# Optimization experiments

Measured on AMD Instinct MI355X. Metric: run time of the kernel, lower is better.

The kernel has to match this reference:

```python
import jax, jax.numpy as jnp
import numpy as np
from jax.scipy.special import logsumexp

S, L = 32768, 512  # seq_len, label_num


def setup_inputs() -> dict:
    key = jax.random.key(0)
    k1, k2, k3 = jax.random.split(key, 3)
    logit = jax.random.normal(k1, (S, L), dtype=jnp.float32)   # emissions [S, L]
    labels = jax.random.randint(k2, (S,), 0, L)                # gold path [S]
    T = jax.random.normal(k3, (L, L), dtype=jnp.float32)       # T[next, prev]
    return {"logit": logit, "labels": labels, "T": T}


def _crf_loss(logit, T, labels):
    # Forward algorithm: alpha_t[j] = logsumexp_i(alpha_{t-1}[i] + T[j, i]) + feat_t[j]
    alpha0 = logit[0]

    def step(alpha, feat):
        new_alpha = logsumexp(alpha[None, :] + T, axis=1) + feat  # [L]
        return new_alpha, None

    alpha_final, _ = jax.lax.scan(step, alpha0, logit[1:])
    log_Z = logsumexp(alpha_final)

    # Gold path score: feat_0[y0] + sum_{t>0} (feat_t[y_t] + T[y_t, y_{t-1}])
    emit = logit[0, labels[0]] + jnp.sum(logit[jnp.arange(1, logit.shape[0]), labels[1:]])
    trans = jnp.sum(T[labels[1:], labels[:-1]])
    gold = emit + trans
    return log_Z - gold


def reference(logit, labels, T):
    return _crf_loss(logit, T, labels)
```

## Files before the change

kernel.cpp:

```cpp
#include <hip/hip_runtime.h>
#include <stdint.h>


#define S_LEN 32768
#define L 512
#define CH 16
#define NCF 2048
#define WGF 128
#define WGB 128
#define LN448 6.104793232f
#define LN2   0.6931471806f

#define OFF_EAF  0
#define OFF_EAB  (256*1024)
#define OFF_G    (512*1024)
#define OFF_H    (OFF_G + 2048*512*2)
#define OFF_LSE  (OFF_H + 2048*512*2)
#define OFF_GOLD (OFF_LSE + 4104*4)

typedef float v4f __attribute__((ext_vector_type(4)));

__device__ __forceinline__ float b2f(unsigned short u){
  return __uint_as_float(((unsigned)u) << 16);
}
__device__ __forceinline__ unsigned short f2b(float x){
  unsigned u = __float_as_uint(x);
  return (unsigned short)((u + 0x7fffu + ((u >> 16) & 1u)) >> 16);
}
__device__ __forceinline__ unsigned char to_fp8(float v){
  int u = __builtin_amdgcn_cvt_pk_fp8_f32(v, v, 0, false);
  return (unsigned char)(u & 0xff);
}

extern "C" __global__ void crf_prep(const float* __restrict__ T,
                                    unsigned char* __restrict__ EAf,
                                    unsigned char* __restrict__ EAb){
  int tid = blockIdx.x*512 + threadIdx.x;
  int r    = tid & 7;
  int lane = (tid >> 3) & 63;
  int kt   = (tid >> 9) & 15;
  int mtw  = tid >> 13;
  int j = (mtw >> 2)*64 + (mtw & 3)*16 + (lane & 15);
  int i = kt*32 + ((lane >> 4) << 3) + r;
  EAf[tid] = to_fp8(2.0f * __expf(T[j*L + i]));
  EAb[tid] = to_fp8(2.0f * __expf(T[i*L + j]));
}

extern "C" __global__ __launch_bounds__(512, 2)
void crf_chunks(const float* __restrict__ logit,
                const unsigned char* __restrict__ EAf,
                const unsigned char* __restrict__ EAb,
                unsigned short* __restrict__ G, unsigned short* __restrict__ H){
  __shared__ __align__(16) unsigned char Pl[2][8192];
  __shared__ float sPart[16][8];

  const int tid  = threadIdx.x;
  const int w    = tid >> 6;
  const int lane = tid & 63;
  const int quad = lane >> 4;
  const int cl   = lane & 15;
  const bool fwd = (blockIdx.x < WGF);
  const int  b   = fwd ? blockIdx.x : (blockIdx.x - WGF);
  const int  cg  = fwd ? (b*16 + cl) : (1 + b*16 + cl);
  const int  cgc = min(cg, NCF-1);
  const bool isc0 = fwd && (cg == 0);
  const int  jrow0 = w*64 + quad*4;

  const long* EA = (const long*)(fwd ? EAf : EAb);
  long eA[4][16];
  #pragma unroll
  for (int mt = 0; mt < 4; ++mt)
    #pragma unroll
    for (int kt = 0; kt < 16; ++kt)
      eA[mt][kt] = EA[(((w<<2)+mt)<<4 | kt)*64 + lane];

  float vr[4][4];
  if (fwd) {
    #pragma unroll
    for (int mt = 0; mt < 4; ++mt)
      #pragma unroll
      for (int r = 0; r < 4; ++r) vr[mt][r] = 1.0f;
  } else {
    const int t0 = cgc*CH + CH - 1;
    const float* lp = logit + (size_t)t0*L + jrow0;
    #pragma unroll
    for (int mt = 0; mt < 4; ++mt) {
      float4 x = *(const float4*)(lp + mt*16);
      vr[mt][0] = __expf(x.x); vr[mt][1] = __expf(x.y);
      vr[mt][2] = __expf(x.z); vr[mt][3] = __expf(x.w);
    }
  }
  float m = 0.0f;
  int par = 0;

  auto renorm_store = [&](int dst){
    float mx = vr[0][0];
    #pragma unroll
    for (int mt = 0; mt < 4; ++mt)
      #pragma unroll
      for (int r = 0; r < 4; ++r) mx = fmaxf(mx, vr[mt][r]);
    mx = fmaxf(mx, __shfl_xor(mx, 16));
    mx = fmaxf(mx, __shfl_xor(mx, 32));
    if (quad == 0) sPart[cl][w] = mx;
    __syncthreads();
    float4 pa = *(const float4*)&sPart[cl][0];
    float4 pb = *(const float4*)&sPart[cl][4];
    float M = fmaxf(fmaxf(fmaxf(pa.x,pa.y),fmaxf(pa.z,pa.w)),
                    fmaxf(fmaxf(pb.x,pb.y),fmaxf(pb.z,pb.w)));
    float sc = 448.0f / M;
    #pragma unroll
    for (int mt = 0; mt < 4; ++mt) {
      int u = __builtin_amdgcn_cvt_pk_fp8_f32(vr[mt][0]*sc, vr[mt][1]*sc, 0, false);
      u     = __builtin_amdgcn_cvt_pk_fp8_f32(vr[mt][2]*sc, vr[mt][3]*sc, u, true);
      int r0 = jrow0 + mt*16;
      *(int*)&Pl[dst][(r0 >> 5)*512 + ((((r0 >> 3) & 3)*16 + cl) << 3) + (r0 & 7)] = u;
    }
    m += __logf(M) - LN448;
    __syncthreads();
  };

  renorm_store(0);

  for (int k = 0; k < CH; ++k) {
    const bool last = (k == CH-1);
    const bool useF = fwd || !last;

    v4f acc[4];
    #pragma unroll
    for (int mt = 0; mt < 4; ++mt) acc[mt] = (v4f){0.f,0.f,0.f,0.f};
    #pragma unroll
    for (int kt = 0; kt < 16; ++kt) {
      long bb = *(const long*)&Pl[par][kt*512 + lane*8];
      #pragma unroll
      for (int mt = 0; mt < 4; ++mt)
        acc[mt] = __builtin_amdgcn_mfma_f32_16x16x32_fp8_fp8(eA[mt][kt], bb, acc[mt], 0, 0, 0);
    }
    m -= LN2;

    if (useF) {
      const int t = fwd ? (cgc*CH + k) : (cgc*CH + CH - 2 - k);
      const float* lp = logit + (size_t)t*L + jrow0;
      #pragma unroll
      for (int mt = 0; mt < 4; ++mt) {
        float4 x = *(const float4*)(lp + mt*16);
        float f0 = __expf(x.x), f1 = __expf(x.y), f2 = __expf(x.z), f3 = __expf(x.w);
        vr[mt][0] = acc[mt][0]*f0; vr[mt][1] = acc[mt][1]*f1;
        vr[mt][2] = acc[mt][2]*f2; vr[mt][3] = acc[mt][3]*f3;
        if (k == 0 && isc0) {
          vr[mt][0] = f0; vr[mt][1] = f1; vr[mt][2] = f2; vr[mt][3] = f3;
        }
      }
      if (k == 0 && isc0) m = 0.0f;
    } else {
      #pragma unroll
      for (int mt = 0; mt < 4; ++mt)
        #pragma unroll
        for (int r = 0; r < 4; ++r) vr[mt][r] = acc[mt][r];
    }

    if (last) {
      if (cg <= NCF-1) {
        unsigned short* dst = (fwd ? G : H) + (size_t)cg*L + jrow0;
        #pragma unroll
        for (int mt = 0; mt < 4; ++mt) {
          ushort4 o;
          o.x = f2b(__logf(vr[mt][0]) + m); o.y = f2b(__logf(vr[mt][1]) + m);
          o.z = f2b(__logf(vr[mt][2]) + m); o.w = f2b(__logf(vr[mt][3]) + m);
          *(ushort4*)(dst + mt*16) = o;
        }
      }
    } else {
      renorm_store(par ^ 1);
      par ^= 1;
    }
  }
}

__device__ __forceinline__ float blockMax(float v, float* sred){
  #pragma unroll
  for (int off = 32; off >= 1; off >>= 1) v = fmaxf(v, __shfl_xor(v, off));
  int wid = threadIdx.x >> 6, lane = threadIdx.x & 63;
  if (lane == 0) sred[wid] = v;
  __syncthreads();
  if (threadIdx.x < 8) {
    float t = sred[threadIdx.x];
    t = fmaxf(t, __shfl_xor(t, 4));
    t = fmaxf(t, __shfl_xor(t, 2));
    t = fmaxf(t, __shfl_xor(t, 1));
    if (threadIdx.x == 0) sred[15] = t;
  }
  __syncthreads();
  float r = sred[15];
  __syncthreads();
  return r;
}
__device__ __forceinline__ float blockSum(float v, float* sred){
  #pragma unroll
  for (int off = 32; off >= 1; off >>= 1) v += __shfl_xor(v, off);
  int wid = threadIdx.x >> 6, lane = threadIdx.x & 63;
  if (lane == 0) sred[wid] = v;
  __syncthreads();
  if (threadIdx.x < 8) {
    float t = sred[threadIdx.x];
    t += __shfl_xor(t, 4); t += __shfl_xor(t, 2); t += __shfl_xor(t, 1);
    if (threadIdx.x == 0) sred[15] = t;
  }
  __syncthreads();
  float r = sred[15];
  __syncthreads();
  return r;
}

extern "C" __global__ __launch_bounds__(512)
void crf_lse(const unsigned short* __restrict__ G,
             const unsigned short* __restrict__ H,
             float* __restrict__ lsebuf){
  __shared__ float sred[16];
  int j = threadIdx.x, b = blockIdx.x;
  if (b == 0) {
    float v = b2f(G[(size_t)(NCF-1)*L + j]);
    float M = blockMax(v, sred);
    float ss = blockSum(__expf(v - M), sred);
    if (j == 0) lsebuf[2*NCF] = M + __logf(ss);
  } else {
    int c = b;
    float h = b2f(H[(size_t)c*L + j]);
    float g = b2f(G[(size_t)(c-1)*L + j]);
    float v1 = h + g;
    float M1 = blockMax(v1, sred);
    float s1 = blockSum(__expf(v1 - M1), sred);
    float M2 = blockMax(h, sred);
    float s2 = blockSum(__expf(h - M2), sred);
    if (j == 0) { lsebuf[c] = M1 + __logf(s1); lsebuf[NCF + c] = M2 + __logf(s2); }
  }
}

extern "C" __global__ void crf_gold(const float* __restrict__ logit,
                                    const int* __restrict__ labels,
                                    const float* __restrict__ T,
                                    float* __restrict__ part){
  __shared__ float sred[8];
  int tid = threadIdx.x;
  float acc = 0.f;
  for (int t = blockIdx.x*256 + tid; t < S_LEN; t += gridDim.x*256) {
    int yt = labels[t];
    float v = logit[(size_t)t*L + yt];
    if (t > 0) v += T[yt*L + labels[t-1]];
    acc += v;
  }
  #pragma unroll
  for (int off = 32; off >= 1; off >>= 1) acc += __shfl_xor(acc, off);
  int wid = tid >> 6, lane = tid & 63;
  if (lane == 0) sred[wid] = acc;
  __syncthreads();
  if (tid == 0) part[blockIdx.x] = sred[0] + sred[1] + sred[2] + sred[3];
}

extern "C" __global__ __launch_bounds__(512)
void crf_final(const float* __restrict__ lsebuf,
               const float* __restrict__ part,
               float* __restrict__ out){
  __shared__ float sred[16];
  int j = threadIdx.x;
  float acc = 0.f;
  #pragma unroll
  for (int c = j; c < NCF; c += 512)
    if (c >= 1) acc += lsebuf[c] - lsebuf[NCF + c];
  if (j < 64) acc -= part[j];
  float s = blockSum(acc, sred);
  if (j == 0) out[0] = lsebuf[2*NCF] + s;
}

extern "C" void kernel_launch(void* const* d_in, const int* in_sizes, int n_in,
                              void* d_out, int out_size, void* d_ws, size_t ws_size,
                              hipStream_t stream){
  const float* logit = (const float*)d_in[0];
  const int* labels  = (const int*)d_in[1];
  const float* T     = (const float*)d_in[2];
  float* out = (float*)d_out;
  char* ws = (char*)d_ws;
  unsigned char* EAf = (unsigned char*)(ws + OFF_EAF);
  unsigned char* EAb = (unsigned char*)(ws + OFF_EAB);
  unsigned short* G  = (unsigned short*)(ws + OFF_G);
  unsigned short* H  = (unsigned short*)(ws + OFF_H);
  float* lsebuf = (float*)(ws + OFF_LSE);
  float* part   = (float*)(ws + OFF_GOLD);

  crf_prep  <<<512, 512, 0, stream>>>(T, EAf, EAb);
  crf_chunks<<<WGF + WGB, 512, 0, stream>>>(logit, EAf, EAb, G, H);
  crf_lse   <<<NCF, 512, 0, stream>>>(G, H, lsebuf);
  crf_gold  <<<64, 256, 0, stream>>>(logit, labels, T, part);
  crf_final <<<1, 512, 0, stream>>>(lsebuf, part, out);
}
```

Before: 148.8 us.

## Fuse CRF pipeline into one persistent kernel with grid barriers

```diff
diff --git a/kernel.cpp b/kernel.cpp
--- a/kernel.cpp
+++ b/kernel.cpp
@@ -6,8 +6,7 @@
 #define L 512
 #define CH 16
 #define NCF 2048
-#define WGF 128
-#define WGB 128
+#define NB  256
 #define LN448 6.104793232f
 #define LN2   0.6931471806f
 
@@ -17,6 +16,7 @@
 #define OFF_H    (OFF_G + 2048*512*2)
 #define OFF_LSE  (OFF_H + 2048*512*2)
 #define OFF_GOLD (OFF_LSE + 4104*4)
+#define OFF_BAR  (OFF_GOLD + 1024)
 
 typedef float v4f __attribute__((ext_vector_type(4)));
 
@@ -32,168 +32,17 @@
   return (unsigned char)(u & 0xff);
 }
 
-extern "C" __global__ void crf_prep(const float* __restrict__ T,
-                                    unsigned char* __restrict__ EAf,
-                                    unsigned char* __restrict__ EAb){
-  int tid = blockIdx.x*512 + threadIdx.x;
-  int r    = tid & 7;
-  int lane = (tid >> 3) & 63;
-  int kt   = (tid >> 9) & 15;
-  int mtw  = tid >> 13;
-  int j = (mtw >> 2)*64 + (mtw & 3)*16 + (lane & 15);
-  int i = kt*32 + ((lane >> 4) << 3) + r;
-  EAf[tid] = to_fp8(2.0f * __expf(T[j*L + i]));
-  EAb[tid] = to_fp8(2.0f * __expf(T[i*L + j]));
-}
-
-extern "C" __global__ __launch_bounds__(512, 2)
-void crf_chunks(const float* __restrict__ logit,
-                const unsigned char* __restrict__ EAf,
-                const unsigned char* __restrict__ EAb,
-                unsigned short* __restrict__ G, unsigned short* __restrict__ H){
-  __shared__ __align__(16) unsigned char Pl[2][8192];
-  __shared__ float sPart[16][8];
-
-  const int tid  = threadIdx.x;
-  const int w    = tid >> 6;
-  const int lane = tid & 63;
-  const int quad = lane >> 4;
-  const int cl   = lane & 15;
-  const bool fwd = (blockIdx.x < WGF);
-  const int  b   = fwd ? blockIdx.x : (blockIdx.x - WGF);
-  const int  cg  = fwd ? (b*16 + cl) : (1 + b*16 + cl);
-  const int  cgc = min(cg, NCF-1);
-  const bool isc0 = fwd && (cg == 0);
-  const int  jrow0 = w*64 + quad*4;
-
-  const long* EA = (const long*)(fwd ? EAf : EAb);
-  long eA[4][16];
-  #pragma unroll
-  for (int mt = 0; mt < 4; ++mt)
-    #pragma unroll
-    for (int kt = 0; kt < 16; ++kt)
-      eA[mt][kt] = EA[(((w<<2)+mt)<<4 | kt)*64 + lane];
-
-  float vr[4][4];
-  if (fwd) {
-    #pragma unroll
-    for (int mt = 0; mt < 4; ++mt)
-      #pragma unroll
-      for (int r = 0; r < 4; ++r) vr[mt][r] = 1.0f;
-  } else {
-    const int t0 = cgc*CH + CH - 1;
-    const float* lp = logit + (size_t)t0*L + jrow0;
-    #pragma unroll
-    for (int mt = 0; mt < 4; ++mt) {
-      float4 x = *(const float4*)(lp + mt*16);
-      vr[mt][0] = __expf(x.x); vr[mt][1] = __expf(x.y);
-      vr[mt][2] = __expf(x.z); vr[mt][3] = __expf(x.w);
-    }
-  }
-  float m = 0.0f;
-  int par = 0;
-
-  auto renorm_store = [&](int dst){
-    float mx = vr[0][0];
-    #pragma unroll
-    for (int mt = 0; mt < 4; ++mt)
-      #pragma unroll
-      for (int r = 0; r < 4; ++r) mx = fmaxf(mx, vr[mt][r]);
-    mx = fmaxf(mx, __shfl_xor(mx, 16));
-    mx = fmaxf(mx, __shfl_xor(mx, 32));
-    if (quad == 0) sPart[cl][w] = mx;
-    __syncthreads();
-    float4 pa = *(const float4*)&sPart[cl][0];
-    float4 pb = *(const float4*)&sPart[cl][4];
-    float M = fmaxf(fmaxf(fmaxf(pa.x,pa.y),fmaxf(pa.z,pa.w)),
-                    fmaxf(fmaxf(pb.x,pb.y),fmaxf(pb.z,pb.w)));
-    float sc = 448.0f / M;
-    #pragma unroll
-    for (int mt = 0; mt < 4; ++mt) {
-      int u = __builtin_amdgcn_cvt_pk_fp8_f32(vr[mt][0]*sc, vr[mt][1]*sc, 0, false);
-      u     = __builtin_amdgcn_cvt_pk_fp8_f32(vr[mt][2]*sc, vr[mt][3]*sc, u, true);
-      int r0 = jrow0 + mt*16;
-      *(int*)&Pl[dst][(r0 >> 5)*512 + ((((r0 >> 3) & 3)*16 + cl) << 3) + (r0 & 7)] = u;
-    }
-    m += __logf(M) - LN448;
-    __syncthreads();
-  };
-
-  renorm_store(0);
-
-  for (int k = 0; k < CH; ++k) {
-    const bool last = (k == CH-1);
-    const bool useF = fwd || !last;
-
-    v4f acc[4];
-    #pragma unroll
-    for (int mt = 0; mt < 4; ++mt) acc[mt] = (v4f){0.f,0.f,0.f,0.f};
-    #pragma unroll
-    for (int kt = 0; kt < 16; ++kt) {
-      long bb = *(const long*)&Pl[par][kt*512 + lane*8];
-      #pragma unroll
-      for (int mt = 0; mt < 4; ++mt)
-        acc[mt] = __builtin_amdgcn_mfma_f32_16x16x32_fp8_fp8(eA[mt][kt], bb, acc[mt], 0, 0, 0);
-    }
-    m -= LN2;
-
-    if (useF) {
-      const int t = fwd ? (cgc*CH + k) : (cgc*CH + CH - 2 - k);
-      const float* lp = logit + (size_t)t*L + jrow0;
-      #pragma unroll
-      for (int mt = 0; mt < 4; ++mt) {
-        float4 x = *(const float4*)(lp + mt*16);
-        float f0 = __expf(x.x), f1 = __expf(x.y), f2 = __expf(x.z), f3 = __expf(x.w);
-        vr[mt][0] = acc[mt][0]*f0; vr[mt][1] = acc[mt][1]*f1;
-        vr[mt][2] = acc[mt][2]*f2; vr[mt][3] = acc[mt][3]*f3;
-        if (k == 0 && isc0) {
-          vr[mt][0] = f0; vr[mt][1] = f1; vr[mt][2] = f2; vr[mt][3] = f3;
-        }
-      }
-      if (k == 0 && isc0) m = 0.0f;
-    } else {
-      #pragma unroll
-      for (int mt = 0; mt < 4; ++mt)
-        #pragma unroll
-        for (int r = 0; r < 4; ++r) vr[mt][r] = acc[mt][r];
-    }
-
-    if (last) {
-      if (cg <= NCF-1) {
-        unsigned short* dst = (fwd ? G : H) + (size_t)cg*L + jrow0;
-        #pragma unroll
-        for (int mt = 0; mt < 4; ++mt) {
-          ushort4 o;
-          o.x = f2b(__logf(vr[mt][0]) + m); o.y = f2b(__logf(vr[mt][1]) + m);
-          o.z = f2b(__logf(vr[mt][2]) + m); o.w = f2b(__logf(vr[mt][3]) + m);
-          *(ushort4*)(dst + mt*16) = o;
-        }
-      }
-    } else {
-      renorm_store(par ^ 1);
-      par ^= 1;
-    }
-  }
-}
-
-__device__ __forceinline__ float blockMax(float v, float* sred){
-  #pragma unroll
-  for (int off = 32; off >= 1; off >>= 1) v = fmaxf(v, __shfl_xor(v, off));
-  int wid = threadIdx.x >> 6, lane = threadIdx.x & 63;
-  if (lane == 0) sred[wid] = v;
-  __syncthreads();
-  if (threadIdx.x < 8) {
-    float t = sred[threadIdx.x];
-    t = fmaxf(t, __shfl_xor(t, 4));
-    t = fmaxf(t, __shfl_xor(t, 2));
-    t = fmaxf(t, __shfl_xor(t, 1));
-    if (threadIdx.x == 0) sred[15] = t;
-  }
-  __syncthreads();
-  float r = sred[15];
-  __syncthreads();
-  return r;
-}
+__device__ __forceinline__ void grid_bar(unsigned* bar, unsigned target){
+  __syncthreads();
+  if (threadIdx.x == 0) {
+    __threadfence();
+    __hip_atomic_fetch_add(bar, 1u, __ATOMIC_RELEASE, __HIP_MEMORY_SCOPE_AGENT);
+    while (__hip_atomic_load(bar, __ATOMIC_ACQUIRE, __HIP_MEMORY_SCOPE_AGENT) < target)
+      __builtin_amdgcn_s_sleep(2);
+  }
+  __syncthreads();
+}
+
 __device__ __forceinline__ float blockSum(float v, float* sred){
   #pragma unroll
   for (int off = 32; off >= 1; off >>= 1) v += __shfl_xor(v, off);
@@ -211,64 +60,246 @@
   return r;
 }
 
-extern "C" __global__ __launch_bounds__(512)
-void crf_lse(const unsigned short* __restrict__ G,
-             const unsigned short* __restrict__ H,
-             float* __restrict__ lsebuf){
-  __shared__ float sred[16];
-  int j = threadIdx.x, b = blockIdx.x;
-  if (b == 0) {
-    float v = b2f(G[(size_t)(NCF-1)*L + j]);
-    float M = blockMax(v, sred);
-    float ss = blockSum(__expf(v - M), sred);
-    if (j == 0) lsebuf[2*NCF] = M + __logf(ss);
-  } else {
-    int c = b;
-    float h = b2f(H[(size_t)c*L + j]);
-    float g = b2f(G[(size_t)(c-1)*L + j]);
-    float v1 = h + g;
-    float M1 = blockMax(v1, sred);
-    float s1 = blockSum(__expf(v1 - M1), sred);
-    float M2 = blockMax(h, sred);
-    float s2 = blockSum(__expf(h - M2), sred);
-    if (j == 0) { lsebuf[c] = M1 + __logf(s1); lsebuf[NCF + c] = M2 + __logf(s2); }
-  }
-}
-
-extern "C" __global__ void crf_gold(const float* __restrict__ logit,
-                                    const int* __restrict__ labels,
-                                    const float* __restrict__ T,
-                                    float* __restrict__ part){
-  __shared__ float sred[8];
-  int tid = threadIdx.x;
-  float acc = 0.f;
-  for (int t = blockIdx.x*256 + tid; t < S_LEN; t += gridDim.x*256) {
-    int yt = labels[t];
-    float v = logit[(size_t)t*L + yt];
-    if (t > 0) v += T[yt*L + labels[t-1]];
-    acc += v;
-  }
+__device__ __forceinline__ float waveMax(float v){
   #pragma unroll
-  for (int off = 32; off >= 1; off >>= 1) acc += __shfl_xor(acc, off);
-  int wid = tid >> 6, lane = tid & 63;
-  if (lane == 0) sred[wid] = acc;
-  __syncthreads();
-  if (tid == 0) part[blockIdx.x] = sred[0] + sred[1] + sred[2] + sred[3];
-}
-
-extern "C" __global__ __launch_bounds__(512)
-void crf_final(const float* __restrict__ lsebuf,
-               const float* __restrict__ part,
-               float* __restrict__ out){
-  __shared__ float sred[16];
-  int j = threadIdx.x;
-  float acc = 0.f;
+  for (int off = 32; off >= 1; off >>= 1) v = fmaxf(v, __shfl_xor(v, off));
+  return v;
+}
+__device__ __forceinline__ float waveSum(float v){
   #pragma unroll
-  for (int c = j; c < NCF; c += 512)
-    if (c >= 1) acc += lsebuf[c] - lsebuf[NCF + c];
-  if (j < 64) acc -= part[j];
-  float s = blockSum(acc, sred);
-  if (j == 0) out[0] = lsebuf[2*NCF] + s;
+  for (int off = 32; off >= 1; off >>= 1) v += __shfl_xor(v, off);
+  return v;
+}
+
+extern "C" __global__ __launch_bounds__(512, 2)
+void crf_fused(const float* __restrict__ logit,
+               const int* __restrict__ labels,
+               const float* __restrict__ T,
+               float* __restrict__ out,
+               unsigned char* __restrict__ EAf,
+               unsigned char* __restrict__ EAb,
+               unsigned short* __restrict__ G,
+               unsigned short* __restrict__ H,
+               float* __restrict__ lsebuf,
+               float* __restrict__ part,
+               unsigned* __restrict__ bar){
+  __shared__ __align__(16) unsigned char Pl[2][8192];
+  __shared__ float sPart[16][8];
+  __shared__ float sredG[16];
+
+  const int tidx = threadIdx.x;
+
+  for (int tid = blockIdx.x*512 + tidx; tid < 262144; tid += NB*512) {
+    int r    = tid & 7;
+    int lane = (tid >> 3) & 63;
+    int kt   = (tid >> 9) & 15;
+    int mtw  = tid >> 13;
+    int j = (mtw >> 2)*64 + (mtw & 3)*16 + (lane & 15);
+    int i = kt*32 + ((lane >> 4) << 3) + r;
+    EAf[tid] = to_fp8(2.0f * __expf(T[j*L + i]));
+    EAb[tid] = to_fp8(2.0f * __expf(T[i*L + j]));
+  }
+  {
+    float acc = 0.f;
+    if (tidx < 128) {
+      int t = blockIdx.x*128 + tidx;
+      int yt = labels[t];
+      float v = logit[(size_t)t*L + yt];
+      if (t > 0) v += T[yt*L + labels[t-1]];
+      acc = v;
+    }
+    float s = blockSum(acc, sredG);
+    if (tidx == 0) part[blockIdx.x] = s;
+  }
+  grid_bar(bar, NB);
+
+  {
+    const int w    = tidx >> 6;
+    const int lane = tidx & 63;
+    const int quad = lane >> 4;
+    const int cl   = lane & 15;
+    const bool fwd = (blockIdx.x < NB/2);
+    const int  b   = fwd ? blockIdx.x : (blockIdx.x - NB/2);
+    const int  cg  = fwd ? (b*16 + cl) : (1 + b*16 + cl);
+    const int  cgc = min(cg, NCF-1);
+    const bool isc0 = fwd && (cg == 0);
+    const int  jrow0 = w*64 + quad*4;
+
+    const long* EA = (const long*)(fwd ? EAf : EAb);
+    long eA[4][16];
+    #pragma unroll
+    for (int mt = 0; mt < 4; ++mt)
+      #pragma unroll
+      for (int kt = 0; kt < 16; ++kt)
+        eA[mt][kt] = EA[(((w<<2)+mt)<<4 | kt)*64 + lane];
+
+    float vr[4][4];
+    if (fwd) {
+      #pragma unroll
+      for (int mt = 0; mt < 4; ++mt)
+        #pragma unroll
+        for (int r = 0; r < 4; ++r) vr[mt][r] = 1.0f;
+    } else {
+      const int t0 = cgc*CH + CH - 1;
+      const float* lp = logit + (size_t)t0*L + jrow0;
+      #pragma unroll
+      for (int mt = 0; mt < 4; ++mt) {
+        float4 x = *(const float4*)(lp + mt*16);
+        vr[mt][0] = __expf(x.x); vr[mt][1] = __expf(x.y);
+        vr[mt][2] = __expf(x.z); vr[mt][3] = __expf(x.w);
+      }
+    }
+    float m = 0.0f;
+    int par = 0;
+
+    auto renorm_store = [&](int dst){
+      float mx = vr[0][0];
+      #pragma unroll
+      for (int mt = 0; mt < 4; ++mt)
+        #pragma unroll
+        for (int r = 0; r < 4; ++r) mx = fmaxf(mx, vr[mt][r]);
+      mx = fmaxf(mx, __shfl_xor(mx, 16));
+      mx = fmaxf(mx, __shfl_xor(mx, 32));
+      if (quad == 0) sPart[cl][w] = mx;
+      __syncthreads();
+      float4 pa = *(const float4*)&sPart[cl][0];
+      float4 pb = *(const float4*)&sPart[cl][4];
+      float M = fmaxf(fmaxf(fmaxf(pa.x,pa.y),fmaxf(pa.z,pa.w)),
+                      fmaxf(fmaxf(pb.x,pb.y),fmaxf(pb.z,pb.w)));
+      float sc = 448.0f / M;
+      #pragma unroll
+      for (int mt = 0; mt < 4; ++mt) {
+        int u = __builtin_amdgcn_cvt_pk_fp8_f32(vr[mt][0]*sc, vr[mt][1]*sc, 0, false);
+        u     = __builtin_amdgcn_cvt_pk_fp8_f32(vr[mt][2]*sc, vr[mt][3]*sc, u, true);
+        int r0 = jrow0 + mt*16;
+        *(int*)&Pl[dst][(r0 >> 5)*512 + ((((r0 >> 3) & 3)*16 + cl) << 3) + (r0 & 7)] = u;
+      }
+      m += __logf(M) - LN448;
+      __syncthreads();
+    };
+
+    renorm_store(0);
+
+    for (int k = 0; k < CH; ++k) {
+      const bool last = (k == CH-1);
+      const bool useF = fwd || !last;
+
+      float4 pf[4];
+      if (useF) {
+        const int t = fwd ? (cgc*CH + k) : (cgc*CH + CH - 2 - k);
+        const float* lp = logit + (size_t)t*L + jrow0;
+        #pragma unroll
+        for (int mt = 0; mt < 4; ++mt) pf[mt] = *(const float4*)(lp + mt*16);
+      }
+
+      v4f acc[4];
+      #pragma unroll
+      for (int mt = 0; mt < 4; ++mt) acc[mt] = (v4f){0.f,0.f,0.f,0.f};
+      #pragma unroll
+      for (int kt = 0; kt < 16; ++kt) {
+        long bb = *(const long*)&Pl[par][kt*512 + lane*8];
+        #pragma unroll
+        for (int mt = 0; mt < 4; ++mt)
+          acc[mt] = __builtin_amdgcn_mfma_f32_16x16x32_fp8_fp8(eA[mt][kt], bb, acc[mt], 0, 0, 0);
+      }
+      m -= LN2;
+
+      if (useF) {
+        #pragma unroll
+        for (int mt = 0; mt < 4; ++mt) {
+          float f0 = __expf(pf[mt].x), f1 = __expf(pf[mt].y);
+          float f2 = __expf(pf[mt].z), f3 = __expf(pf[mt].w);
+          vr[mt][0] = acc[mt][0]*f0; vr[mt][1] = acc[mt][1]*f1;
+          vr[mt][2] = acc[mt][2]*f2; vr[mt][3] = acc[mt][3]*f3;
+          if (k == 0 && isc0) {
+            vr[mt][0] = f0; vr[mt][1] = f1; vr[mt][2] = f2; vr[mt][3] = f3;
+          }
+        }
+        if (k == 0 && isc0) m = 0.0f;
+      } else {
+        #pragma unroll
+        for (int mt = 0; mt < 4; ++mt)
+          #pragma unroll
+          for (int r = 0; r < 4; ++r) vr[mt][r] = acc[mt][r];
+      }
+
+      if (last) {
+        if (cg <= NCF-1) {
+          unsigned short* dst = (fwd ? G : H) + (size_t)cg*L + jrow0;
+          #pragma unroll
+          for (int mt = 0; mt < 4; ++mt) {
+            ushort4 o;
+            o.x = f2b(__logf(vr[mt][0]) + m); o.y = f2b(__logf(vr[mt][1]) + m);
+            o.z = f2b(__logf(vr[mt][2]) + m); o.w = f2b(__logf(vr[mt][3]) + m);
+            *(ushort4*)(dst + mt*16) = o;
+          }
+        }
+      } else {
+        renorm_store(par ^ 1);
+        par ^= 1;
+      }
+    }
+  }
+  grid_bar(bar, 2*NB);
+
+  {
+    const int w    = tidx >> 6;
+    const int lane = tidx & 63;
+    const int g    = blockIdx.x*8 + w;
+    const int j8   = lane*8;
+    if (g == 0) {
+      const unsigned short* p = G + (size_t)(NCF-1)*L + j8;
+      ushort4 a = *(const ushort4*)p, b = *(const ushort4*)(p + 4);
+      float v[8] = { b2f(a.x),b2f(a.y),b2f(a.z),b2f(a.w),
+                     b2f(b.x),b2f(b.y),b2f(b.z),b2f(b.w) };
+      float mx = v[0];
+      #pragma unroll
+      for (int r = 1; r < 8; ++r) mx = fmaxf(mx, v[r]);
+      mx = waveMax(mx);
+      float s = 0.f;
+      #pragma unroll
+      for (int r = 0; r < 8; ++r) s += __expf(v[r] - mx);
+      s = waveSum(s);
+      if (lane == 0) lsebuf[2*NCF] = mx + __logf(s);
+    } else {
+      const unsigned short* hp = H + (size_t)g*L + j8;
+      const unsigned short* gp = G + (size_t)(g-1)*L + j8;
+      ushort4 ha = *(const ushort4*)hp, hb = *(const ushort4*)(hp + 4);
+      ushort4 ga = *(const ushort4*)gp, gb = *(const ushort4*)(gp + 4);
+      float hv[8] = { b2f(ha.x),b2f(ha.y),b2f(ha.z),b2f(ha.w),
+                      b2f(hb.x),b2f(hb.y),b2f(hb.z),b2f(hb.w) };
+      float gv[8] = { b2f(ga.x),b2f(ga.y),b2f(ga.z),b2f(ga.w),
+                      b2f(gb.x),b2f(gb.y),b2f(gb.z),b2f(gb.w) };
+      float m1 = -3.0e38f, m2 = -3.0e38f;
+      #pragma unroll
+      for (int r = 0; r < 8; ++r) {
+        float a = hv[r] + gv[r];
+        m1 = fmaxf(m1, a); m2 = fmaxf(m2, hv[r]);
+      }
+      m1 = waveMax(m1); m2 = waveMax(m2);
+      float s1 = 0.f, s2 = 0.f;
+      #pragma unroll
+      for (int r = 0; r < 8; ++r) {
+        s1 += __expf(hv[r] + gv[r] - m1);
+        s2 += __expf(hv[r] - m2);
+      }
+      s1 = waveSum(s1); s2 = waveSum(s2);
+      if (lane == 0) {
+        lsebuf[g]       = m1 + __logf(s1);
+        lsebuf[NCF + g] = m2 + __logf(s2);
+      }
+    }
+  }
+  grid_bar(bar, 3*NB);
+
+  if (blockIdx.x == 0) {
+    float acc = 0.f;
+    for (int c = tidx; c < NCF; c += 512)
+      if (c >= 1) acc += lsebuf[c] - lsebuf[NCF + c];
+    if (tidx < NB) acc -= part[tidx];
+    float s = blockSum(acc, sredG);
+    if (tidx == 0) out[0] = lsebuf[2*NCF] + s;
+  }
 }
 
 extern "C" void kernel_launch(void* const* d_in, const int* in_sizes, int n_in,
@@ -277,18 +308,13 @@
   const float* logit = (const float*)d_in[0];
   const int* labels  = (const int*)d_in[1];
   const float* T     = (const float*)d_in[2];
-  float* out = (float*)d_out;
   char* ws = (char*)d_ws;
-  unsigned char* EAf = (unsigned char*)(ws + OFF_EAF);
-  unsigned char* EAb = (unsigned char*)(ws + OFF_EAB);
-  unsigned short* G  = (unsigned short*)(ws + OFF_G);
-  unsigned short* H  = (unsigned short*)(ws + OFF_H);
-  float* lsebuf = (float*)(ws + OFF_LSE);
-  float* part   = (float*)(ws + OFF_GOLD);
-
-  crf_prep  <<<512, 512, 0, stream>>>(T, EAf, EAb);
-  crf_chunks<<<WGF + WGB, 512, 0, stream>>>(logit, EAf, EAb, G, H);
-  crf_lse   <<<NCF, 512, 0, stream>>>(G, H, lsebuf);
-  crf_gold  <<<64, 256, 0, stream>>>(logit, labels, T, part);
-  crf_final <<<1, 512, 0, stream>>>(lsebuf, part, out);
-}
+
+  hipMemsetAsync(ws + OFF_BAR, 0, 64, stream);
+  crf_fused<<<NB, 512, 0, stream>>>(
+      logit, labels, T, (float*)d_out,
+      (unsigned char*)(ws + OFF_EAF), (unsigned char*)(ws + OFF_EAB),
+      (unsigned short*)(ws + OFF_G), (unsigned short*)(ws + OFF_H),
+      (float*)(ws + OFF_LSE), (float*)(ws + OFF_GOLD),
+      (unsigned*)(ws + OFF_BAR));
+}
```

Measured after the change: 200.8 us. 1.35x slower.
